# Kernel optimization log

Measured on AMD Instinct MI355X. Metric: run time of the kernel, lower is better.

## Reference

```python
import math
import jax, jax.numpy as jnp
import numpy as np

B, S, D_MODEL, NUM_HEADS = 4, 2048, 1024, 16
D_N = D_MODEL // NUM_HEADS  # 64


def setup_inputs() -> dict:
    key = jax.random.key(0)
    ks = jax.random.split(key, 10)
    scale = 1.0 / math.sqrt(D_MODEL)
    return {
        "q": jax.random.normal(ks[0], (B, S, D_MODEL), dtype=jnp.float32),
        "k": jax.random.normal(ks[1], (B, S, D_MODEL), dtype=jnp.float32),
        "v": jax.random.normal(ks[2], (B, S, D_MODEL), dtype=jnp.float32),
        "mask": jax.random.uniform(ks[3], (B, S, S), dtype=jnp.float32),
        "w_q": jax.random.normal(ks[4], (D_N, D_MODEL), dtype=jnp.float32) * scale,
        "b_q": jnp.zeros((D_N,), dtype=jnp.float32),
        "w_k": jax.random.normal(ks[5], (D_N, D_MODEL), dtype=jnp.float32) * scale,
        "b_k": jnp.zeros((D_N,), dtype=jnp.float32),
        "w_v": jax.random.normal(ks[6], (D_N, D_MODEL), dtype=jnp.float32) * scale,
        "b_v": jnp.zeros((D_N,), dtype=jnp.float32),
    }


def reference(q, k, v, mask, w_q, b_q, w_k, b_k, w_v, b_v):
    # Linear projections d_model -> d_n (torch Linear: x @ W.T + b)
    qp = jnp.einsum("bsd,nd->bsn", q, w_q) + b_q  # [B,S,d_n]
    kp = jnp.einsum("bsd,nd->bsn", k, w_k) + b_k
    vp = jnp.einsum("bsd,nd->bsn", v, w_v) + b_v
    # Scaled dot-product scores with additive mask penalty
    scores = jnp.einsum("bqn,bkn->bqk", qp, kp) / math.sqrt(D_N) + mask * (-1e9)
    attn = jax.nn.softmax(scores, axis=-1)  # [B,S,S]
    return jnp.einsum("bqk,bkn->bqn", attn, vp)  # [B,S,d_n]
```

## Files before the change

### kernel.cpp

```cpp
#include <hip/hip_runtime.h>
#include <hip/hip_bf16.h>

#define BB 4
#define SS 2048
#define DM 1024
#define DN 64

typedef short short8 __attribute__((ext_vector_type(8)));
typedef float f32x4 __attribute__((ext_vector_type(4)));
typedef unsigned short ushort;

__device__ __forceinline__ ushort f2bf(float f) {
    union { float f; unsigned u; } v; v.f = f;
    unsigned r = v.u + 0x7fffu + ((v.u >> 16) & 1u);
    return (ushort)(r >> 16);
}
__device__ __forceinline__ float bf2f(ushort h) {
    union { unsigned u; float f; } v; v.u = ((unsigned)h) << 16; return v.f;
}

__global__ __launch_bounds__(256) void prep_w(
    const float* __restrict__ wq, const float* __restrict__ wk,
    const float* __restrict__ wv, ushort* __restrict__ w_bf)
{
    int i = blockIdx.x * 256 + threadIdx.x;
    int p = i >> 14;
    int j = (i & 16383) * 4;
    const float* src = (p == 0) ? wq : (p == 1) ? wk : wv;
    float4 f = *(const float4*)(src + j);
    ushort o[4] = { f2bf(f.x), f2bf(f.y), f2bf(f.z), f2bf(f.w) };
    *(unsigned long long*)(w_bf + p * 65536 + j) = *(unsigned long long*)o;
}

__global__ __launch_bounds__(128, 2) void proj_kernel(
    const float* __restrict__ q, const float* __restrict__ k, const float* __restrict__ v,
    const ushort* __restrict__ w_bf,
    const float* __restrict__ bq, const float* __restrict__ bk, const float* __restrict__ bvp,
    ushort* __restrict__ qp, ushort* __restrict__ kp, ushort* __restrict__ vpT)
{
    const int tid  = threadIdx.x;
    const int proj = blockIdx.y;
    const int wv_id = tid >> 6;
    const int lane  = tid & 63;
    const int l16   = lane & 15;
    const int quad  = lane >> 4;
    const int g     = blockIdx.x * 2 + wv_id;
    const int m0    = g * 16;

    const float* x     = (proj == 0) ? q  : (proj == 1) ? k  : v;
    const ushort* wb   = w_bf + proj * 65536;
    const float* bias  = (proj == 0) ? bq : (proj == 1) ? bk : bvp;

    const float* arow = x + (size_t)(m0 + l16) * DM + quad * 8;

    f32x4 acc[4];
#pragma unroll
    for (int t = 0; t < 4; t++) acc[t] = (f32x4){0.f, 0.f, 0.f, 0.f};

#pragma unroll 4
    for (int kb = 0; kb < DM; kb += 32) {
        float4 f0 = *(const float4*)(arow + kb);
        float4 f1 = *(const float4*)(arow + kb + 4);
        ushort ta[8] = { f2bf(f0.x), f2bf(f0.y), f2bf(f0.z), f2bf(f0.w),
                         f2bf(f1.x), f2bf(f1.y), f2bf(f1.z), f2bf(f1.w) };
        short8 a = *(short8*)ta;
#pragma unroll
        for (int t = 0; t < 4; t++) {
            short8 b = *(const short8*)(wb + (size_t)(t * 16 + l16) * DM + kb + quad * 8);
            acc[t] = __builtin_amdgcn_mfma_f32_16x16x32_bf16(a, b, acc[t], 0, 0, 0);
        }
    }

#pragma unroll
    for (int t = 0; t < 4; t++) {
        int n = t * 16 + l16;
        float bb_ = bias[n];
#pragma unroll
        for (int r = 0; r < 4; r++) {
            int grow = m0 + quad * 4 + r;
            ushort h = f2bf(acc[t][r] + bb_);
            if (proj == 0)      qp[(size_t)grow * DN + n] = h;
            else if (proj == 1) kp[(size_t)grow * DN + n] = h;
            else {
                int bb = grow >> 11, s = grow & 2047;
                vpT[((size_t)bb * DN + n) * SS + s] = h;
            }
        }
    }
}

template<int KPS>
__global__ __launch_bounds__(256, 2) void flash_kernel(
    const float* __restrict__ mask,
    const ushort* __restrict__ qp,
    const ushort* __restrict__ kp,
    const ushort* __restrict__ vpT,
    ushort* __restrict__ part_O,
    float* __restrict__ part_ml)
{
    constexpr int NSLICE = SS / KPS;
    constexpr int NIT    = KPS / 64;

    __shared__ __align__(16) ushort p_lds[4][16][72];

    const int tid  = threadIdx.x;
    const int wv   = tid >> 6;
    const int lane = tid & 63;
    const int l16  = lane & 15;
    const int quad = lane >> 4;

    const int gw    = blockIdx.x * 4 + wv;
    const int qg    = gw & 127;
    const int rest  = gw >> 7;
    const int slice = rest % NSLICE;
    const int b     = rest / NSLICE;

    const ushort* qbase = qp + ((size_t)b * SS + qg * 16 + l16) * DN + quad * 8;
    short8 aq0 = *(const short8*)(qbase);
    short8 aq1 = *(const short8*)(qbase + 32);

    float m_r[4] = { -__builtin_inff(), -__builtin_inff(),
                     -__builtin_inff(), -__builtin_inff() };
    float l_r[4] = { 0.f, 0.f, 0.f, 0.f };
    f32x4 Oacc[4];
#pragma unroll
    for (int t = 0; t < 4; t++) Oacc[t] = (f32x4){0.f, 0.f, 0.f, 0.f};

    const size_t mrow0 = ((size_t)b * SS + qg * 16 + quad * 4) * SS;
    const int k_begin = slice * KPS;

    float  mk[2][4][4];
    short8 bk0[2][4], bk1[2][4];

    auto load_tile = [&](int buf, int k0) {
#pragma unroll
        for (int t = 0; t < 4; t++) {
            const ushort* kb_ = kp + ((size_t)b * SS + k0 + t * 16 + l16) * DN + quad * 8;
            bk0[buf][t] = *(const short8*)(kb_);
            bk1[buf][t] = *(const short8*)(kb_ + 32);
        }
#pragma unroll
        for (int t = 0; t < 4; t++)
#pragma unroll
            for (int r = 0; r < 4; r++)
                mk[buf][t][r] = mask[mrow0 + (size_t)r * SS + k0 + t * 16 + l16];
    };

    load_tile(0, k_begin);

#pragma unroll
    for (int it = 0; it < NIT; ++it) {
        const int cur = it & 1;
        const int k0  = k_begin + it * 64;

        if (it + 1 < NIT) load_tile(cur ^ 1, k0 + 64);

        short8 bv0[4], bv1[4];
#pragma unroll
        for (int tf = 0; tf < 4; tf++) {
            const ushort* vb_ = vpT + ((size_t)b * DN + tf * 16 + l16) * SS + k0 + quad * 8;
            bv0[tf] = *(const short8*)(vb_);
            bv1[tf] = *(const short8*)(vb_ + 32);
        }

        f32x4 sc[4];
#pragma unroll
        for (int t = 0; t < 4; t++) {
            f32x4 z = (f32x4){0.f, 0.f, 0.f, 0.f};
            z = __builtin_amdgcn_mfma_f32_16x16x32_bf16(aq0, bk0[cur][t], z, 0, 0, 0);
            z = __builtin_amdgcn_mfma_f32_16x16x32_bf16(aq1, bk1[cur][t], z, 0, 0, 0);
            sc[t] = z;
        }

#pragma unroll
        for (int r = 0; r < 4; r++) {
            float s[4];
            float tmax = -__builtin_inff();
#pragma unroll
            for (int t = 0; t < 4; t++) {
                s[t] = sc[t][r] * 0.125f - 1e9f * mk[cur][t][r];
                tmax = fmaxf(tmax, s[t]);
            }
#pragma unroll
            for (int off = 8; off >= 1; off >>= 1)
                tmax = fmaxf(tmax, __shfl_xor(tmax, off, 16));
            float mnew  = fmaxf(m_r[r], tmax);
            float alpha = __expf(m_r[r] - mnew);
            m_r[r] = mnew;
            float rs = 0.f;
#pragma unroll
            for (int t = 0; t < 4; t++) {
                float pv = __expf(s[t] - mnew);
                rs += pv;
                p_lds[wv][quad * 4 + r][t * 16 + l16] = f2bf(pv);
            }
#pragma unroll
            for (int off = 8; off >= 1; off >>= 1)
                rs += __shfl_xor(rs, off, 16);
            l_r[r] = l_r[r] * alpha + rs;
#pragma unroll
            for (int tf = 0; tf < 4; tf++)
                Oacc[tf][r] *= alpha;
        }

        short8 ap0 = *(const short8*)&p_lds[wv][l16][quad * 8];
        short8 ap1 = *(const short8*)&p_lds[wv][l16][32 + quad * 8];
#pragma unroll
        for (int tf = 0; tf < 4; tf++) {
            Oacc[tf] = __builtin_amdgcn_mfma_f32_16x16x32_bf16(ap0, bv0[tf], Oacc[tf], 0, 0, 0);
            Oacc[tf] = __builtin_amdgcn_mfma_f32_16x16x32_bf16(ap1, bv1[tf], Oacc[tf], 0, 0, 0);
        }
    }

    const int rowg = (b * SS + qg * 16) + quad * 4;
#pragma unroll
    for (int r = 0; r < 4; r++) {
        size_t row = (size_t)rowg + r;
        if (l16 == 0) {
            part_ml[((size_t)slice * (BB * SS) + row) * 2 + 0] = m_r[r];
            part_ml[((size_t)slice * (BB * SS) + row) * 2 + 1] = l_r[r];
        }
#pragma unroll
        for (int tf = 0; tf < 4; tf++)
            part_O[((size_t)slice * (BB * SS) + row) * DN + tf * 16 + l16] =
                f2bf(Oacc[tf][r]);
    }
}

__global__ __launch_bounds__(256) void combine_kernel(
    const ushort* __restrict__ part_O, const float* __restrict__ part_ml,
    float* __restrict__ out, int nslice)
{
    const int tid = threadIdx.x;
    const int row = blockIdx.x * 4 + (tid >> 6);
    const int f   = tid & 63;

    float ms[8], ls[8];
    float M = -__builtin_inff();
    for (int i = 0; i < nslice; i++) {
        ms[i] = part_ml[((size_t)i * (BB * SS) + row) * 2 + 0];
        ls[i] = part_ml[((size_t)i * (BB * SS) + row) * 2 + 1];
        M = fmaxf(M, ms[i]);
    }
    float L = 0.f, acc = 0.f;
    for (int i = 0; i < nslice; i++) {
        float e = __expf(ms[i] - M);
        L += e * ls[i];
        acc += e * bf2f(part_O[((size_t)i * (BB * SS) + row) * DN + f]);
    }
    out[(size_t)row * DN + f] = acc / L;
}

extern "C" void kernel_launch(void* const* d_in, const int* in_sizes, int n_in,
                              void* d_out, int out_size, void* d_ws, size_t ws_size,
                              hipStream_t stream) {
    const float* q    = (const float*)d_in[0];
    const float* k    = (const float*)d_in[1];
    const float* v    = (const float*)d_in[2];
    const float* mask = (const float*)d_in[3];
    const float* wq   = (const float*)d_in[4];
    const float* bq   = (const float*)d_in[5];
    const float* wk   = (const float*)d_in[6];
    const float* bk   = (const float*)d_in[7];
    const float* wv   = (const float*)d_in[8];
    const float* bv   = (const float*)d_in[9];
    float* out = (float*)d_out;

    char* p = (char*)d_ws;
    ushort* w_bf = (ushort*)p;                 p += 3 * 65536 * sizeof(ushort);
    ushort* qp   = (ushort*)p;                 p += (size_t)BB * SS * DN * 2;
    ushort* kp   = (ushort*)p;                 p += (size_t)BB * SS * DN * 2;
    ushort* vpT  = (ushort*)p;                 p += (size_t)BB * SS * DN * 2;
    size_t fixed = (size_t)(p - (char*)d_ws);

    int split = 8;
    while (split > 1 &&
           fixed + (size_t)split * ((size_t)BB * SS * 2 * 4 + (size_t)BB * SS * DN * 2) > ws_size)
        split >>= 1;

    float*  part_ml = (float*)p;               p += (size_t)split * BB * SS * 2 * 4;
    ushort* part_O  = (ushort*)p;

    prep_w<<<192, 256, 0, stream>>>(wq, wk, wv, w_bf);
    proj_kernel<<<dim3(256, 3), 128, 0, stream>>>(q, k, v, w_bf, bq, bk, bv, qp, kp, vpT);
    switch (split) {
        case 8:  flash_kernel<256> <<<128 * 8, 256, 0, stream>>>(mask, qp, kp, vpT, part_O, part_ml); break;
        case 4:  flash_kernel<512> <<<128 * 4, 256, 0, stream>>>(mask, qp, kp, vpT, part_O, part_ml); break;
        case 2:  flash_kernel<1024><<<128 * 2, 256, 0, stream>>>(mask, qp, kp, vpT, part_O, part_ml); break;
        default: flash_kernel<2048><<<128 * 1, 256, 0, stream>>>(mask, qp, kp, vpT, part_O, part_ml); break;
    }
    combine_kernel<<<(BB * SS) / 4, 256, 0, stream>>>(part_O, part_ml, out, split);
}
```

Before: 240.1 us.

## Split projection GEMM along K with separate reduction kernel

```diff
diff --git a/kernel.cpp b/kernel.cpp
--- a/kernel.cpp
+++ b/kernel.cpp
@@ -32,33 +32,37 @@
     *(unsigned long long*)(w_bf + p * 65536 + j) = *(unsigned long long*)o;
 }
 
-__global__ __launch_bounds__(128, 2) void proj_kernel(
+template<int PS>
+__global__ __launch_bounds__(256) void proj_main(
     const float* __restrict__ q, const float* __restrict__ k, const float* __restrict__ v,
-    const ushort* __restrict__ w_bf,
-    const float* __restrict__ bq, const float* __restrict__ bk, const float* __restrict__ bvp,
-    ushort* __restrict__ qp, ushort* __restrict__ kp, ushort* __restrict__ vpT)
+    const ushort* __restrict__ w_bf, float* __restrict__ part)
 {
     const int tid  = threadIdx.x;
-    const int proj = blockIdx.y;
     const int wv_id = tid >> 6;
     const int lane  = tid & 63;
     const int l16   = lane & 15;
     const int quad  = lane >> 4;
-    const int g     = blockIdx.x * 2 + wv_id;
-    const int m0    = g * 16;
-
-    const float* x     = (proj == 0) ? q  : (proj == 1) ? k  : v;
-    const ushort* wb   = w_bf + proj * 65536;
-    const float* bias  = (proj == 0) ? bq : (proj == 1) ? bk : bvp;
+
+    const int w    = blockIdx.x * 4 + wv_id;
+    const int proj = w / (512 * PS);
+    const int rem  = w % (512 * PS);
+    const int g    = rem / PS;
+    const int slice = rem % PS;
+    const int m0   = g * 16;
+
+    const float* x   = (proj == 0) ? q : (proj == 1) ? k : v;
+    const ushort* wb = w_bf + proj * 65536;
 
     const float* arow = x + (size_t)(m0 + l16) * DM + quad * 8;
+    const int k_begin = slice * (DM / PS);
+    const int k_end   = k_begin + (DM / PS);
 
     f32x4 acc[4];
 #pragma unroll
     for (int t = 0; t < 4; t++) acc[t] = (f32x4){0.f, 0.f, 0.f, 0.f};
 
-#pragma unroll 4
-    for (int kb = 0; kb < DM; kb += 32) {
+#pragma unroll 2
+    for (int kb = k_begin; kb < k_end; kb += 32) {
         float4 f0 = *(const float4*)(arow + kb);
         float4 f1 = *(const float4*)(arow + kb + 4);
         ushort ta[8] = { f2bf(f0.x), f2bf(f0.y), f2bf(f0.z), f2bf(f0.w),
@@ -71,21 +75,35 @@
         }
     }
 
-#pragma unroll
-    for (int t = 0; t < 4; t++) {
-        int n = t * 16 + l16;
-        float bb_ = bias[n];
-#pragma unroll
-        for (int r = 0; r < 4; r++) {
-            int grow = m0 + quad * 4 + r;
-            ushort h = f2bf(acc[t][r] + bb_);
-            if (proj == 0)      qp[(size_t)grow * DN + n] = h;
-            else if (proj == 1) kp[(size_t)grow * DN + n] = h;
-            else {
-                int bb = grow >> 11, s = grow & 2047;
-                vpT[((size_t)bb * DN + n) * SS + s] = h;
-            }
-        }
+    float* pb = part + ((size_t)(proj * PS + slice) * (BB * SS) + m0) * DN;
+#pragma unroll
+    for (int t = 0; t < 4; t++)
+#pragma unroll
+        for (int r = 0; r < 4; r++)
+            pb[(size_t)(quad * 4 + r) * DN + t * 16 + l16] = acc[t][r];
+}
+
+__global__ __launch_bounds__(256) void proj_reduce(
+    const float* __restrict__ part,
+    const float* __restrict__ bq, const float* __restrict__ bk, const float* __restrict__ bvp,
+    ushort* __restrict__ qp, ushort* __restrict__ kp, ushort* __restrict__ vpT, int PS)
+{
+    const int idx  = blockIdx.x * 256 + threadIdx.x;
+    const int proj = idx / (BB * SS * DN);
+    const int rem  = idx % (BB * SS * DN);
+    const int row  = rem >> 6;
+    const int n    = rem & 63;
+
+    const float* bias = (proj == 0) ? bq : (proj == 1) ? bk : bvp;
+    float s = bias[n];
+    for (int i = 0; i < PS; i++)
+        s += part[((size_t)(proj * PS + i) * (BB * SS) + row) * DN + n];
+    ushort h = f2bf(s);
+    if (proj == 0)      qp[(size_t)row * DN + n] = h;
+    else if (proj == 1) kp[(size_t)row * DN + n] = h;
+    else {
+        int bb = row >> 11, ss = row & 2047;
+        vpT[((size_t)bb * DN + n) * SS + ss] = h;
     }
 }
 
@@ -267,22 +285,40 @@
     float* out = (float*)d_out;
 
     char* p = (char*)d_ws;
-    ushort* w_bf = (ushort*)p;                 p += 3 * 65536 * sizeof(ushort);
-    ushort* qp   = (ushort*)p;                 p += (size_t)BB * SS * DN * 2;
-    ushort* kp   = (ushort*)p;                 p += (size_t)BB * SS * DN * 2;
-    ushort* vpT  = (ushort*)p;                 p += (size_t)BB * SS * DN * 2;
+    ushort* w_bf = (ushort*)p;   p += 3 * 65536 * sizeof(ushort);
+    ushort* qp   = (ushort*)p;   p += (size_t)BB * SS * DN * 2;
+    ushort* kp   = (ushort*)p;   p += (size_t)BB * SS * DN * 2;
+    ushort* vpT  = (ushort*)p;   p += (size_t)BB * SS * DN * 2;
     size_t fixed = (size_t)(p - (char*)d_ws);
 
     int split = 8;
-    while (split > 1 &&
-           fixed + (size_t)split * ((size_t)BB * SS * 2 * 4 + (size_t)BB * SS * DN * 2) > ws_size)
+    size_t flash_bytes;
+    for (;;) {
+        flash_bytes = (size_t)split * BB * SS * 2 * 4 + (size_t)split * BB * SS * DN * 2;
+        if (split == 1 || fixed + flash_bytes <= ws_size) break;
         split >>= 1;
-
-    float*  part_ml = (float*)p;               p += (size_t)split * BB * SS * 2 * 4;
-    ushort* part_O  = (ushort*)p;
+    }
+
+    int PS = 4;
+    while (PS > 1) {
+        size_t proj_bytes = (size_t)3 * PS * BB * SS * DN * 4;
+        size_t need = proj_bytes > flash_bytes ? proj_bytes : flash_bytes;
+        if (fixed + need <= ws_size) break;
+        PS >>= 1;
+    }
+
+    float*  proj_part = (float*)p;
+    float*  part_ml   = (float*)p;   p += (size_t)split * BB * SS * 2 * 4;
+    ushort* part_O    = (ushort*)p;
 
     prep_w<<<192, 256, 0, stream>>>(wq, wk, wv, w_bf);
-    proj_kernel<<<dim3(256, 3), 128, 0, stream>>>(q, k, v, w_bf, bq, bk, bv, qp, kp, vpT);
+    switch (PS) {
+        case 4: proj_main<4><<<128 * 3 * 4, 256, 0, stream>>>(q, k, v, w_bf, proj_part); break;
+        case 2: proj_main<2><<<128 * 3 * 2, 256, 0, stream>>>(q, k, v, w_bf, proj_part); break;
+        default: proj_main<1><<<128 * 3, 256, 0, stream>>>(q, k, v, w_bf, proj_part); break;
+    }
+    proj_reduce<<<(3 * BB * SS * DN) / 256, 256, 0, stream>>>(proj_part, bq, bk, bv,
+                                                              qp, kp, vpT, PS);
     switch (split) {
         case 8:  flash_kernel<256> <<<128 * 8, 256, 0, stream>>>(mask, qp, kp, vpT, part_O, part_ml); break;
         case 4:  flash_kernel<512> <<<128 * 4, 256, 0, stream>>>(mask, qp, kp, vpT, part_O, part_ml); break;
```

Measured after the change: 241.0 us. No clear change (+0.4%).

## Stage projection input tiles through LDS with coalesced double-buffered prefetch

Applied to the files above, without the earlier changes.

```diff
diff --git a/kernel.cpp b/kernel.cpp
--- a/kernel.cpp
+++ b/kernel.cpp
@@ -32,58 +32,86 @@
     *(unsigned long long*)(w_bf + p * 65536 + j) = *(unsigned long long*)o;
 }
 
-__global__ __launch_bounds__(128, 2) void proj_kernel(
+__global__ __launch_bounds__(256) void proj_kernel(
     const float* __restrict__ q, const float* __restrict__ k, const float* __restrict__ v,
     const ushort* __restrict__ w_bf,
     const float* __restrict__ bq, const float* __restrict__ bk, const float* __restrict__ bvp,
     ushort* __restrict__ qp, ushort* __restrict__ kp, ushort* __restrict__ vpT)
 {
+    __shared__ __align__(16) ushort A_lds[2][32][136];
+
     const int tid  = threadIdx.x;
     const int proj = blockIdx.y;
-    const int wv_id = tid >> 6;
-    const int lane  = tid & 63;
-    const int l16   = lane & 15;
-    const int quad  = lane >> 4;
-    const int g     = blockIdx.x * 2 + wv_id;
-    const int m0    = g * 16;
-
-    const float* x     = (proj == 0) ? q  : (proj == 1) ? k  : v;
-    const ushort* wb   = w_bf + proj * 65536;
-    const float* bias  = (proj == 0) ? bq : (proj == 1) ? bk : bvp;
-
-    const float* arow = x + (size_t)(m0 + l16) * DM + quad * 8;
-
-    f32x4 acc[4];
-#pragma unroll
-    for (int t = 0; t < 4; t++) acc[t] = (f32x4){0.f, 0.f, 0.f, 0.f};
-
-#pragma unroll 4
-    for (int kb = 0; kb < DM; kb += 32) {
-        float4 f0 = *(const float4*)(arow + kb);
-        float4 f1 = *(const float4*)(arow + kb + 4);
-        ushort ta[8] = { f2bf(f0.x), f2bf(f0.y), f2bf(f0.z), f2bf(f0.w),
-                         f2bf(f1.x), f2bf(f1.y), f2bf(f1.z), f2bf(f1.w) };
-        short8 a = *(short8*)ta;
-#pragma unroll
-        for (int t = 0; t < 4; t++) {
-            short8 b = *(const short8*)(wb + (size_t)(t * 16 + l16) * DM + kb + quad * 8);
-            acc[t] = __builtin_amdgcn_mfma_f32_16x16x32_bf16(a, b, acc[t], 0, 0, 0);
-        }
-    }
-
-#pragma unroll
-    for (int t = 0; t < 4; t++) {
-        int n = t * 16 + l16;
+    const int m0   = blockIdx.x * 32;
+
+    const float* x    = (proj == 0) ? q  : (proj == 1) ? k  : v;
+    const ushort* wb  = w_bf + proj * 65536;
+    const float* bias = (proj == 0) ? bq : (proj == 1) ? bk : bvp;
+
+    const int wv   = tid >> 6;
+    const int lane = tid & 63;
+    const int l16  = lane & 15;
+    const int quad = lane >> 4;
+    const int rg   = wv & 1;
+    const int nh   = wv >> 1;
+
+    const int srow = tid >> 5;
+    const int slc  = tid & 31;
+
+    float4 pf[4];
+    auto issue_loads = [&](int kb) {
+#pragma unroll
+        for (int r = 0; r < 4; r++)
+            pf[r] = *(const float4*)&x[(size_t)(m0 + srow + r * 8) * DM + kb + slc * 4];
+    };
+    auto write_stage = [&](int buf) {
+#pragma unroll
+        for (int r = 0; r < 4; r++) {
+            ushort t4[4] = { f2bf(pf[r].x), f2bf(pf[r].y), f2bf(pf[r].z), f2bf(pf[r].w) };
+            *(unsigned long long*)&A_lds[buf][srow + r * 8][slc * 4] =
+                *(unsigned long long*)t4;
+        }
+    };
+
+    f32x4 acc[2];
+    acc[0] = (f32x4){0.f, 0.f, 0.f, 0.f};
+    acc[1] = (f32x4){0.f, 0.f, 0.f, 0.f};
+
+    issue_loads(0);
+
+#pragma unroll
+    for (int s = 0; s < 8; s++) {
+        const int buf = s & 1;
+        write_stage(buf);
+        if (s < 7) issue_loads((s + 1) * 128);
+        __syncthreads();
+
+        const int kb = s * 128;
+#pragma unroll
+        for (int kk = 0; kk < 128; kk += 32) {
+            short8 a = *(const short8*)&A_lds[buf][rg * 16 + l16][kk + quad * 8];
+#pragma unroll
+            for (int tt = 0; tt < 2; tt++) {
+                const int t = nh * 2 + tt;
+                short8 b = *(const short8*)(wb + (size_t)(t * 16 + l16) * DM + kb + kk + quad * 8);
+                acc[tt] = __builtin_amdgcn_mfma_f32_16x16x32_bf16(a, b, acc[tt], 0, 0, 0);
+            }
+        }
+    }
+
+#pragma unroll
+    for (int tt = 0; tt < 2; tt++) {
+        const int n = (nh * 2 + tt) * 16 + l16;
         float bb_ = bias[n];
 #pragma unroll
         for (int r = 0; r < 4; r++) {
-            int grow = m0 + quad * 4 + r;
-            ushort h = f2bf(acc[t][r] + bb_);
+            int grow = m0 + rg * 16 + quad * 4 + r;
+            ushort h = f2bf(acc[tt][r] + bb_);
             if (proj == 0)      qp[(size_t)grow * DN + n] = h;
             else if (proj == 1) kp[(size_t)grow * DN + n] = h;
             else {
-                int bb = grow >> 11, s = grow & 2047;
-                vpT[((size_t)bb * DN + n) * SS + s] = h;
+                int bb = grow >> 11, ss = grow & 2047;
+                vpT[((size_t)bb * DN + n) * SS + ss] = h;
             }
         }
     }
@@ -267,22 +295,24 @@
     float* out = (float*)d_out;
 
     char* p = (char*)d_ws;
-    ushort* w_bf = (ushort*)p;                 p += 3 * 65536 * sizeof(ushort);
-    ushort* qp   = (ushort*)p;                 p += (size_t)BB * SS * DN * 2;
-    ushort* kp   = (ushort*)p;                 p += (size_t)BB * SS * DN * 2;
-    ushort* vpT  = (ushort*)p;                 p += (size_t)BB * SS * DN * 2;
+    ushort* w_bf = (ushort*)p;   p += 3 * 65536 * sizeof(ushort);
+    ushort* qp   = (ushort*)p;   p += (size_t)BB * SS * DN * 2;
+    ushort* kp   = (ushort*)p;   p += (size_t)BB * SS * DN * 2;
+    ushort* vpT  = (ushort*)p;   p += (size_t)BB * SS * DN * 2;
     size_t fixed = (size_t)(p - (char*)d_ws);
 
     int split = 8;
-    while (split > 1 &&
-           fixed + (size_t)split * ((size_t)BB * SS * 2 * 4 + (size_t)BB * SS * DN * 2) > ws_size)
+    for (;;) {
+        size_t flash_bytes = (size_t)split * BB * SS * 2 * 4 + (size_t)split * BB * SS * DN * 2;
+        if (split == 1 || fixed + flash_bytes <= ws_size) break;
         split >>= 1;
-
-    float*  part_ml = (float*)p;               p += (size_t)split * BB * SS * 2 * 4;
+    }
+
+    float*  part_ml = (float*)p;   p += (size_t)split * BB * SS * 2 * 4;
     ushort* part_O  = (ushort*)p;
 
     prep_w<<<192, 256, 0, stream>>>(wq, wk, wv, w_bf);
-    proj_kernel<<<dim3(256, 3), 128, 0, stream>>>(q, k, v, w_bf, bq, bk, bv, qp, kp, vpT);
+    proj_kernel<<<dim3(256, 3), 256, 0, stream>>>(q, k, v, w_bf, bq, bk, bv, qp, kp, vpT);
     switch (split) {
         case 8:  flash_kernel<256> <<<128 * 8, 256, 0, stream>>>(mask, qp, kp, vpT, part_O, part_ml); break;
         case 4:  flash_kernel<512> <<<128 * 4, 256, 0, stream>>>(mask, qp, kp, vpT, part_O, part_ml); break;
```

Result: faster. 226.9 us (-5.5%).
